# Kernel optimization log

Hardware: AMD Instinct MI355X
Metric: run time of the kernel (lower is better)

## Reference

```python
import jax, jax.numpy as jnp
import numpy as np

B, N, D = 2, 2048, 1024
H, DH = 16, 64
DI = 4096
EPS = 1e-5
NEG_SLOPE = 0.01  # F.leaky_relu default


def _ln(x, g, b):
    mu = jnp.mean(x, axis=-1, keepdims=True)
    var = jnp.mean((x - mu) ** 2, axis=-1, keepdims=True)
    return (x - mu) * jax.lax.rsqrt(var + EPS) * g + b


def setup_inputs() -> dict:
    key = jax.random.key(0)
    ks = jax.random.split(key, 10)
    s = 0.02
    return {
        "Z": jax.random.normal(ks[0], (B, N, D), jnp.float32),
        "new_mask": jax.random.normal(ks[1], (B, N, N), jnp.float32),
        "mask": jax.random.uniform(ks[2], (B, N, N), jnp.float32),
        "ln1_g": jnp.ones((D,), jnp.float32),
        "ln1_b": jnp.zeros((D,), jnp.float32),
        "qkv_w": jax.random.normal(ks[3], (3 * D, D), jnp.float32) * s,
        "qkv_b": jnp.zeros((3 * D,), jnp.float32),
        "o_w": jax.random.normal(ks[4], (D, H * DH), jnp.float32) * s,
        "ln2_g": jnp.ones((D,), jnp.float32),
        "ln2_b": jnp.zeros((D,), jnp.float32),
        "p1_w": jax.random.normal(ks[5], (DI, D), jnp.float32) * s,
        "p1_b": jnp.zeros((DI,), jnp.float32),
        "p2_w": jax.random.normal(ks[6], (D, DI), jnp.float32) * s,
        "p2_b": jnp.zeros((D,), jnp.float32),
    }


def reference(Z, new_mask, mask, ln1_g, ln1_b, qkv_w, qkv_b, o_w, ln2_g, ln2_b, p1_w, p1_b, p2_w, p2_b):
    inp = Z
    Zn = _ln(Z, ln1_g, ln1_b)
    qkv = (Zn @ qkv_w.T + qkv_b).reshape(B, N, H, 3 * DH)
    # torch chunk order in the source: V, Q, K
    V, Q, K = jnp.split(qkv, 3, axis=3)  # each [B,N,H,DH]
    # scores: einsum('bnij,bmij->binm') == [B,H,N,N]
    W = jnp.einsum("bnhd,bmhd->bhnm", Q, K) / np.sqrt(DH) + new_mask[:, None]
    A = jax.nn.softmax(W, axis=3) * mask[:, None]
    attn = jnp.einsum("bhnm,bmhd->bnhd", A, V).reshape(B, N, D)
    attn = jnp.where(attn >= 0, attn, NEG_SLOPE * attn) @ o_w.T  # leaky_relu then o_net (no bias)
    Z1 = attn + inp
    Zn2 = _ln(Z1, ln2_g, ln2_b)
    h = jax.nn.relu(Zn2 @ p1_w.T + p1_b)
    return h @ p2_w.T + p2_b + Z1
```

## Files before the change

### kernel.cpp

```cpp
#include <hip/hip_runtime.h>

typedef unsigned short u16;
typedef __attribute__((ext_vector_type(8))) short bf16x8;
typedef __attribute__((ext_vector_type(4))) float f32x4;

#define DEV static __device__ __forceinline__

DEV u16 f2bf(float f) {
    unsigned u = __float_as_uint(f);
    u += 0x7FFFu + ((u >> 16) & 1u);
    return (u16)(u >> 16);
}

typedef const __attribute__((address_space(1))) void* gas1_t;
typedef __attribute__((address_space(3))) void* gas3_t;

DEV void gl_lds16(const u16* g, u16* l) {
    __builtin_amdgcn_global_load_lds((gas1_t)g, (gas3_t)l, 16, 0, 0);
}

DEV int sw8(int row, int chunk) { return row * 64 + ((chunk ^ (row & 7)) << 3); }

__global__ __launch_bounds__(256) void prep_all(const float* __restrict__ qkv_w,
                                                const float* __restrict__ o_w,
                                                const float* __restrict__ p1_w,
                                                const float* __restrict__ p2_w,
                                                const float* __restrict__ qkv_b,
                                                const float* __restrict__ nm,
                                                const float* __restrict__ pm,
                                                u16* __restrict__ qkvW,
                                                u16* __restrict__ oW,
                                                u16* __restrict__ p1W,
                                                u16* __restrict__ p2W,
                                                float* __restrict__ pbias,
                                                unsigned* __restrict__ Mp) {
    const int bid = blockIdx.x, t = threadIdx.x;
    if (bid < 3072) {
        int i = bid * 256 + t;
        int orow = i >> 8, cc = i & 255;
        int region = orow >> 10, rem = orow & 1023, h = rem >> 6, tt = rem & 63;
        int srow = h * 192 + region * 64 + tt;
        float4 v = ((const float4*)qkv_w)[srow * 256 + cc];
        ushort4 o;
        o.x = f2bf(v.x); o.y = f2bf(v.y); o.z = f2bf(v.z); o.w = f2bf(v.w);
        ((ushort4*)qkvW)[i] = o;
    } else if (bid < 4096) {
        int i = (bid - 3072) * 256 + t;
        float4 v = ((const float4*)o_w)[i];
        ushort4 o;
        o.x = f2bf(v.x); o.y = f2bf(v.y); o.z = f2bf(v.z); o.w = f2bf(v.w);
        ((ushort4*)oW)[i] = o;
    } else if (bid < 8192) {
        int i = (bid - 4096) * 256 + t;
        float4 v = ((const float4*)p1_w)[i];
        ushort4 o;
        o.x = f2bf(v.x); o.y = f2bf(v.y); o.z = f2bf(v.z); o.w = f2bf(v.w);
        ((ushort4*)p1W)[i] = o;
    } else if (bid < 12288) {
        int i = (bid - 8192) * 256 + t;
        float4 v = ((const float4*)p2_w)[i];
        ushort4 o;
        o.x = f2bf(v.x); o.y = f2bf(v.y); o.z = f2bf(v.z); o.w = f2bf(v.w);
        ((ushort4*)p2W)[i] = o;
    } else if (bid < 20480) {
        int i = (bid - 12288) * 256 + t;
        float4 a = ((const float4*)nm)[i];
        float4 b = ((const float4*)pm)[i];
        uint4 o;
        o.x = ((unsigned)f2bf(b.x) << 16) | f2bf(a.x * 1.4426950f);
        o.y = ((unsigned)f2bf(b.y) << 16) | f2bf(a.y * 1.4426950f);
        o.z = ((unsigned)f2bf(b.z) << 16) | f2bf(a.z * 1.4426950f);
        o.w = ((unsigned)f2bf(b.w) << 16) | f2bf(a.w * 1.4426950f);
        ((uint4*)Mp)[i] = o;
    } else {
#pragma unroll
        for (int k = 0; k < 12; k++) {
            int i = k * 256 + t;
            int region = i >> 10, rem = i & 1023, h = rem >> 6, tt = rem & 63;
            pbias[i] = qkv_b[h * 192 + region * 64 + tt];
        }
    }
}

__global__ __launch_bounds__(256) void ln_bf16(const float* __restrict__ x,
                                               const float* __restrict__ gam,
                                               const float* __restrict__ bet,
                                               u16* __restrict__ y) {
    const int row = blockIdx.x;
    const int t = threadIdx.x;
    const float4 v = ((const float4*)(x + (size_t)row * 1024))[t];
    float s = v.x + v.y + v.z + v.w;
    float ss = v.x * v.x + v.y * v.y + v.z * v.z + v.w * v.w;
#pragma unroll
    for (int o = 1; o < 64; o <<= 1) {
        s += __shfl_xor(s, o);
        ss += __shfl_xor(ss, o);
    }
    __shared__ float rs[4], rss[4];
    const int wave = t >> 6, lane = t & 63;
    if (lane == 0) { rs[wave] = s; rss[wave] = ss; }
    __syncthreads();
    const float tot = rs[0] + rs[1] + rs[2] + rs[3];
    const float totss = rss[0] + rss[1] + rss[2] + rss[3];
    const float mu = tot * (1.0f / 1024.0f);
    const float var = totss * (1.0f / 1024.0f) - mu * mu;
    const float rstd = rsqrtf(var + 1e-5f);
    const float4 g4 = ((const float4*)gam)[t];
    const float4 b4 = ((const float4*)bet)[t];
    ushort4 o;
    o.x = f2bf((v.x - mu) * rstd * g4.x + b4.x);
    o.y = f2bf((v.y - mu) * rstd * g4.y + b4.y);
    o.z = f2bf((v.z - mu) * rstd * g4.z + b4.z);
    o.w = f2bf((v.w - mu) * rstd * g4.w + b4.w);
    ((ushort4*)(y + (size_t)row * 1024))[t] = o;
}

__global__ __launch_bounds__(256) void ln2_comb4(const float* __restrict__ p0,
                                                 const float* __restrict__ p1,
                                                 const float* __restrict__ p2,
                                                 const float* __restrict__ p3,
                                                 const float* __restrict__ Z,
                                                 const float* __restrict__ gam,
                                                 const float* __restrict__ bet,
                                                 float* __restrict__ Z1,
                                                 u16* __restrict__ y) {
    const int row = blockIdx.x;
    const int t = threadIdx.x;
    const size_t off = (size_t)row * 256 + t;
    const float4 a = ((const float4*)p0)[off];
    const float4 c = ((const float4*)p1)[off];
    const float4 d = ((const float4*)p2)[off];
    const float4 e = ((const float4*)p3)[off];
    const float4 z = ((const float4*)Z)[off];
    float4 v;
    v.x = a.x + c.x + d.x + e.x + z.x;
    v.y = a.y + c.y + d.y + e.y + z.y;
    v.z = a.z + c.z + d.z + e.z + z.z;
    v.w = a.w + c.w + d.w + e.w + z.w;
    ((float4*)Z1)[off] = v;
    float s = v.x + v.y + v.z + v.w;
    float ss = v.x * v.x + v.y * v.y + v.z * v.z + v.w * v.w;
#pragma unroll
    for (int o = 1; o < 64; o <<= 1) {
        s += __shfl_xor(s, o);
        ss += __shfl_xor(ss, o);
    }
    __shared__ float rs[4], rss[4];
    const int wave = t >> 6, lane = t & 63;
    if (lane == 0) { rs[wave] = s; rss[wave] = ss; }
    __syncthreads();
    const float tot = rs[0] + rs[1] + rs[2] + rs[3];
    const float totss = rss[0] + rss[1] + rss[2] + rss[3];
    const float mu = tot * (1.0f / 1024.0f);
    const float var = totss * (1.0f / 1024.0f) - mu * mu;
    const float rstd = rsqrtf(var + 1e-5f);
    const float4 g4 = ((const float4*)gam)[t];
    const float4 b4 = ((const float4*)bet)[t];
    ushort4 o;
    o.x = f2bf((v.x - mu) * rstd * g4.x + b4.x);
    o.y = f2bf((v.y - mu) * rstd * g4.y + b4.y);
    o.z = f2bf((v.z - mu) * rstd * g4.z + b4.z);
    o.w = f2bf((v.w - mu) * rstd * g4.w + b4.w);
    ((ushort4*)(y + (size_t)row * 1024))[t] = o;
}

__global__ __launch_bounds__(256) void out_comb(const float* __restrict__ p0,
                                                const float* __restrict__ p1,
                                                const float* __restrict__ bias,
                                                const float* __restrict__ Z1,
                                                float* __restrict__ out) {
    int i = blockIdx.x * 256 + threadIdx.x;
    float4 a = ((const float4*)p0)[i];
    float4 c = ((const float4*)p1)[i];
    float4 z = ((const float4*)Z1)[i];
    float4 b = ((const float4*)bias)[i & 255];
    float4 o;
    o.x = a.x + c.x + z.x + b.x; o.y = a.y + c.y + z.y + b.y;
    o.z = a.z + c.z + z.z + b.z; o.w = a.w + c.w + z.w + b.w;
    ((float4*)out)[i] = o;
}

template <int EPI>
__global__ __launch_bounds__(256, 3) void gemm_bt(const u16* __restrict__ A,
                                                  const u16* __restrict__ Bt,
                                                  const float* __restrict__ bias,
                                                  void* __restrict__ out0,
                                                  void* __restrict__ out1,
                                                  void* __restrict__ out2,
                                                  int M, int N, int K, int ldk) {
    __shared__ __align__(16) u16 As[128 * 32];
    __shared__ __align__(16) u16 Bs[128 * 32];
    const int tid = threadIdx.x;
    const int wave = tid >> 6, lane = tid & 63;
    const int lhi = lane >> 4, llo = lane & 15;
    const int bx = blockIdx.x, by = blockIdx.y;
    const int kz = blockIdx.z * K;

    const int arow = wave * 32 + (lane >> 2);
    const int acol = (lane & 3) * 8;
    const u16* gA = A + (size_t)(by * 128 + arow) * ldk + kz + acol;
    const u16* gB = Bt + (size_t)(bx * 128 + arow) * ldk + kz + acol;
    u16* lA = As + wave * 1024 + lane * 8;
    u16* lB = Bs + wave * 1024 + lane * 8;

    const int wr = wave >> 1, wc = wave & 1;
    const f32x4 zero = {0.f, 0.f, 0.f, 0.f};
    f32x4 acc[4][4];
#pragma unroll
    for (int i = 0; i < 4; i++)
#pragma unroll
        for (int j = 0; j < 4; j++) acc[i][j] = zero;

    for (int k0 = 0; k0 < K; k0 += 32) {
        __syncthreads();
        gl_lds16(gA, lA);
        gl_lds16(gA + 16 * (size_t)ldk, lA + 512);
        gl_lds16(gB, lB);
        gl_lds16(gB + 16 * (size_t)ldk, lB + 512);
        gA += 32; gB += 32;
        __syncthreads();
        bf16x8 af[4], bfr[4];
#pragma unroll
        for (int i = 0; i < 4; i++)
            af[i] = *(const bf16x8*)(As + (wr * 64 + i * 16 + llo) * 32 + lhi * 8);
#pragma unroll
        for (int j = 0; j < 4; j++)
            bfr[j] = *(const bf16x8*)(Bs + (wc * 64 + j * 16 + llo) * 32 + lhi * 8);
#pragma unroll
        for (int i = 0; i < 4; i++)
#pragma unroll
            for (int j = 0; j < 4; j++)
                acc[i][j] = __builtin_amdgcn_mfma_f32_16x16x32_bf16(af[i], bfr[j], acc[i][j], 0, 0, 0);
    }

    const int rbase = by * 128 + wr * 64 + lhi * 4;
    const int cbase = bx * 128 + wc * 64 + llo;
    float* pout = nullptr;
    if constexpr (EPI == 4) {
        pout = (blockIdx.z < 2) ? ((float*)out0 + (size_t)blockIdx.z * M * N)
                                : ((float*)out1 + (size_t)(blockIdx.z - 2) * M * N);
    }
#pragma unroll
    for (int i = 0; i < 4; i++) {
#pragma unroll
        for (int j = 0; j < 4; j++) {
#pragma unroll
            for (int r = 0; r < 4; r++) {
                const int row = rbase + i * 16 + r;
                const int col = cbase + j * 16;
                float v = acc[i][j][r];
                if constexpr (EPI == 0) {
                    v += bias[col];
                    const int region = col >> 10;
                    const int c = col & 1023;
                    const int b = row >> 11, n = row & 2047;
                    if (region == 0) {
                        ((float*)out0)[(size_t)row * 1024 + c] = v;
                    } else {
                        const int h = c >> 6, t = c & 63;
                        u16* dst = (region == 1) ? (u16*)out1 : (u16*)out2;
                        dst[(((size_t)(b * 16 + h)) * 2048 + n) * 64 + t] = f2bf(v);
                    }
                } else if constexpr (EPI == 2) {
                    v += bias[col];
                    v = v > 0.f ? v : 0.f;
                    ((u16*)out0)[(size_t)row * N + col] = f2bf(v);
                } else {
                    pout[(size_t)row * N + col] = v;
                }
            }
        }
    }
}

__global__ __launch_bounds__(256) void vtrans(const float* __restrict__ Vsc,
                                              u16* __restrict__ Vt) {
    __shared__ u16 Ts[64 * 72];
    const int nt = blockIdx.x;
    const int bh = blockIdx.y;
    const int b = bh >> 4, h = bh & 15;
    const int t = threadIdx.x;
    const int n0 = nt * 64;
    const int nr = t >> 2;
    const int dq = (t & 3) * 16;
    const float* src = Vsc + ((size_t)(b * 2048 + n0 + nr)) * 1024 + h * 64 + dq;
    float4 v0 = ((const float4*)src)[0];
    float4 v1 = ((const float4*)src)[1];
    float4 v2 = ((const float4*)src)[2];
    float4 v3 = ((const float4*)src)[3];
    u16* c0 = Ts + nr;
    c0[(dq + 0) * 72]  = f2bf(v0.x); c0[(dq + 1) * 72]  = f2bf(v0.y);
    c0[(dq + 2) * 72]  = f2bf(v0.z); c0[(dq + 3) * 72]  = f2bf(v0.w);
    c0[(dq + 4) * 72]  = f2bf(v1.x); c0[(dq + 5) * 72]  = f2bf(v1.y);
    c0[(dq + 6) * 72]  = f2bf(v1.z); c0[(dq + 7) * 72]  = f2bf(v1.w);
    c0[(dq + 8) * 72]  = f2bf(v2.x); c0[(dq + 9) * 72]  = f2bf(v2.y);
    c0[(dq + 10) * 72] = f2bf(v2.z); c0[(dq + 11) * 72] = f2bf(v2.w);
    c0[(dq + 12) * 72] = f2bf(v3.x); c0[(dq + 13) * 72] = f2bf(v3.y);
    c0[(dq + 14) * 72] = f2bf(v3.z); c0[(dq + 15) * 72] = f2bf(v3.w);
    __syncthreads();
    const int d = t >> 2, n8 = (t & 3) * 16;
    bf16x8 o0 = *(const bf16x8*)(Ts + d * 72 + n8);
    bf16x8 o1 = *(const bf16x8*)(Ts + d * 72 + n8 + 8);
    u16* dst = Vt + ((size_t)bh * 64 + d) * 2048 + n0 + n8;
    *(bf16x8*)dst = o0;
    *(bf16x8*)(dst + 8) = o1;
}

__global__ __launch_bounds__(256, 4) void attn_fused4(const u16* __restrict__ Qg,
                                                      const u16* __restrict__ Kg,
                                                      const u16* __restrict__ Vt,
                                                      const unsigned* __restrict__ Mp,
                                                      u16* __restrict__ attnL) {
    __shared__ __align__(16) u16 Qs[64 * 64];
    __shared__ __align__(16) u16 Ks[64 * 64];
    __shared__ __align__(16) u16 Vs[64 * 64];
    __shared__ __align__(16) u16 Ps[64 * 72];
    const int tid = threadIdx.x, wave = tid >> 6, lane = tid & 63;
    const int lhi = lane >> 4, llo = lane & 15;
    const int id = blockIdx.x;
    const int hh = id >> 6, rem = id & 63;
    const int b = rem >> 5, qt = rem & 31;
    const int bh = b * 16 + hh;
    const int q0 = qt * 64;
    const int l3 = lane >> 3, l7 = lane & 7;
    const int swcol = (l7 ^ (l3 & 7)) * 8;

#pragma unroll
    for (int s = 0; s < 2; s++) {
        const int row = wave * 16 + s * 8 + l3;
        gl_lds16(Qg + ((size_t)bh * 2048 + q0 + row) * 64 + swcol,
                 Qs + wave * 1024 + s * 512 + lane * 8);
    }

    const unsigned* Mpb = Mp + (size_t)b * 2048 * 2048;
    int midx[4];
#pragma unroll
    for (int r = 0; r < 4; r++)
        midx[r] = (q0 + wave * 16 + lhi * 4 + r) * 2048 + llo;

    const f32x4 zero = {0.f, 0.f, 0.f, 0.f};
    f32x4 accO[4];
    float lsum[4];
#pragma unroll
    for (int j = 0; j < 4; j++) accO[j] = zero;
#pragma unroll
    for (int r = 0; r < 4; r++) lsum[r] = 0.f;

    const float CS = 0.125f * 1.4426950f;
    const int pb0 = (wave * 16 + lhi * 4) * 72 + llo;

    for (int m0 = 0; m0 < 2048; m0 += 64) {
        __syncthreads();
#pragma unroll
        for (int s = 0; s < 2; s++) {
            const int row = wave * 16 + s * 8 + l3;
            gl_lds16(Kg + ((size_t)bh * 2048 + m0 + row) * 64 + swcol,
                     Ks + wave * 1024 + s * 512 + lane * 8);
            gl_lds16(Vt + ((size_t)bh * 64 + row) * 2048 + m0 + swcol,
                     Vs + wave * 1024 + s * 512 + lane * 8);
        }
        unsigned mv[4][4];
#pragma unroll
        for (int r = 0; r < 4; r++)
#pragma unroll
            for (int j = 0; j < 4; j++) mv[r][j] = Mpb[midx[r] + m0 + j * 16];
        __syncthreads();

        f32x4 sacc[4];
#pragma unroll
        for (int j = 0; j < 4; j++) sacc[j] = zero;
#pragma unroll
        for (int kk = 0; kk < 2; kk++) {
            const bf16x8 aq = *(const bf16x8*)(Qs + sw8(wave * 16 + llo, kk * 4 + lhi));
#pragma unroll
            for (int j = 0; j < 4; j++) {
                const bf16x8 bk = *(const bf16x8*)(Ks + sw8(j * 16 + llo, kk * 4 + lhi));
                sacc[j] = __builtin_amdgcn_mfma_f32_16x16x32_bf16(aq, bk, sacc[j], 0, 0, 0);
            }
        }

#pragma unroll
        for (int j = 0; j < 4; j++)
#pragma unroll
            for (int r = 0; r < 4; r++) {
                const unsigned u = mv[r][j];
                const float nm = __uint_as_float(u << 16);
                const float pm = __uint_as_float(u & 0xFFFF0000u);
                const float e = exp2f(fmaf(sacc[j][r], CS, nm));
                lsum[r] += e;
                const float p = e * pm;
                Ps[pb0 + r * 72 + j * 16] = (u16)(__float_as_uint(p) >> 16);
            }

#pragma unroll
        for (int kk = 0; kk < 2; kk++) {
            const bf16x8 ap = *(const bf16x8*)(Ps + (wave * 16 + llo) * 72 + kk * 32 + lhi * 8);
#pragma unroll
            for (int jd = 0; jd < 4; jd++) {
                const bf16x8 bv = *(const bf16x8*)(Vs + sw8(jd * 16 + llo, kk * 4 + lhi));
                accO[jd] = __builtin_amdgcn_mfma_f32_16x16x32_bf16(ap, bv, accO[jd], 0, 0, 0);
            }
        }
    }

#pragma unroll
    for (int r = 0; r < 4; r++) {
#pragma unroll
        for (int o = 1; o < 16; o <<= 1) lsum[r] += __shfl_xor(lsum[r], o);
        lsum[r] = 1.0f / lsum[r];
    }
#pragma unroll
    for (int jd = 0; jd < 4; jd++)
#pragma unroll
        for (int r = 0; r < 4; r++) {
            float v = accO[jd][r] * lsum[r];
            v = v >= 0.f ? v : 0.01f * v;
            const int q = q0 + wave * 16 + lhi * 4 + r;
            attnL[((size_t)b * 2048 + q) * 1024 + hh * 64 + jd * 16 + llo] = f2bf(v);
        }
}

extern "C" void kernel_launch(void* const* d_in, const int* in_sizes, int n_in,
                              void* d_out, int out_size, void* d_ws, size_t ws_size,
                              hipStream_t stream) {
    const float* Z     = (const float*)d_in[0];
    const float* nmask = (const float*)d_in[1];
    const float* pmask = (const float*)d_in[2];
    const float* ln1_g = (const float*)d_in[3];
    const float* ln1_b = (const float*)d_in[4];
    const float* qkv_w = (const float*)d_in[5];
    const float* qkv_b = (const float*)d_in[6];
    const float* o_w   = (const float*)d_in[7];
    const float* ln2_g = (const float*)d_in[8];
    const float* ln2_b = (const float*)d_in[9];
    const float* p1_w  = (const float*)d_in[10];
    const float* p1_b  = (const float*)d_in[11];
    const float* p2_w  = (const float*)d_in[12];
    const float* p2_b  = (const float*)d_in[13];
    float* out = (float*)d_out;

    char* w = (char*)d_ws;
    auto take = [&](size_t bytes) -> char* {
        char* p = w;
        w += (bytes + 255) & ~(size_t)255;
        return p;
    };
    u16* qkvW   = (u16*)take((size_t)3072 * 1024 * 2);
    u16* oW     = (u16*)take((size_t)1024 * 1024 * 2);
    u16* p1W    = (u16*)take((size_t)4096 * 1024 * 2);
    u16* p2W    = (u16*)take((size_t)1024 * 4096 * 2);
    u16* Zn     = (u16*)take((size_t)4096 * 1024 * 2);
    u16* Qb     = (u16*)take((size_t)32 * 2048 * 64 * 2);
    u16* Kb     = (u16*)take((size_t)32 * 2048 * 64 * 2);
    u16* Vt     = (u16*)take((size_t)32 * 64 * 2048 * 2);
    u16* attnL  = (u16*)take((size_t)4096 * 1024 * 2);
    float* Z1   = (float*)take((size_t)4096 * 1024 * 4);
    u16* hbuf   = (u16*)take((size_t)4096 * 4096 * 2);
    unsigned* Mp = (unsigned*)take((size_t)2 * 2048 * 2048 * 4);
    float* pbias = (float*)take((size_t)3072 * 4);
    float* Vsc    = (float*)hbuf;
    float* part01 = (float*)Mp;
    float* part23 = (float*)hbuf;

    prep_all<<<dim3(20481), 256, 0, stream>>>(qkv_w, o_w, p1_w, p2_w, qkv_b, nmask, pmask,
                                              qkvW, oW, p1W, p2W, pbias, Mp);
    ln_bf16<<<dim3(4096), 256, 0, stream>>>(Z, ln1_g, ln1_b, Zn);
    gemm_bt<0><<<dim3(24, 32), 256, 0, stream>>>(Zn, qkvW, pbias, Vsc, Qb, Kb, 4096, 3072, 1024, 1024);
    vtrans<<<dim3(32, 32), 256, 0, stream>>>(Vsc, Vt);
    attn_fused4<<<dim3(1024), 256, 0, stream>>>(Qb, Kb, Vt, Mp, attnL);
    gemm_bt<4><<<dim3(8, 32, 4), 256, 0, stream>>>(attnL, oW, nullptr, part01, part23, nullptr,
                                                   4096, 1024, 256, 1024);
    ln2_comb4<<<dim3(4096), 256, 0, stream>>>(part01, part01 + (size_t)4096 * 1024,
                                              part23, part23 + (size_t)4096 * 1024,
                                              Z, ln2_g, ln2_b, Z1, Zn);
    gemm_bt<2><<<dim3(32, 32), 256, 0, stream>>>(Zn, p1W, p1_b, hbuf, nullptr, nullptr,
                                                 4096, 4096, 1024, 1024);
    gemm_bt<4><<<dim3(8, 32, 2), 256, 0, stream>>>(hbuf, p2W, nullptr, part01, nullptr, nullptr,
                                                   4096, 1024, 2048, 4096);
    out_comb<<<dim3(4096), 256, 0, stream>>>(part01, part01 + (size_t)4096 * 1024, p2_b, Z1, out);
}
```

Baseline: 443.8 us.

## Fold LN1 into prep, transpose mask layout, fuse residual into o-proj GEMM

LayerNorm1 now runs inside the prep kernel, which removes one launch. The prep kernel also writes the packed mask transposed, so the attention kernel can load four query rows with one uint4 instead of scattered scalars. The o-projection drops its 4-way split-K and uses a 128x64 tile GEMM that adds the residual in its epilogue, removing the partial-sum combine kernel. V is now written as bf16 to cut vtrans traffic, and the attention exp uses the hardware exp2 builtin. The transposed mask write needs an extra LDS transpose, and the o-proj GEMM now runs a full K loop per block with less parallelism.

```diff
diff --git a/kernel.cpp b/kernel.cpp
--- a/kernel.cpp
+++ b/kernel.cpp
@@ -21,74 +21,8 @@
 
 DEV int sw8(int row, int chunk) { return row * 64 + ((chunk ^ (row & 7)) << 3); }
 
-__global__ __launch_bounds__(256) void prep_all(const float* __restrict__ qkv_w,
-                                                const float* __restrict__ o_w,
-                                                const float* __restrict__ p1_w,
-                                                const float* __restrict__ p2_w,
-                                                const float* __restrict__ qkv_b,
-                                                const float* __restrict__ nm,
-                                                const float* __restrict__ pm,
-                                                u16* __restrict__ qkvW,
-                                                u16* __restrict__ oW,
-                                                u16* __restrict__ p1W,
-                                                u16* __restrict__ p2W,
-                                                float* __restrict__ pbias,
-                                                unsigned* __restrict__ Mp) {
-    const int bid = blockIdx.x, t = threadIdx.x;
-    if (bid < 3072) {
-        int i = bid * 256 + t;
-        int orow = i >> 8, cc = i & 255;
-        int region = orow >> 10, rem = orow & 1023, h = rem >> 6, tt = rem & 63;
-        int srow = h * 192 + region * 64 + tt;
-        float4 v = ((const float4*)qkv_w)[srow * 256 + cc];
-        ushort4 o;
-        o.x = f2bf(v.x); o.y = f2bf(v.y); o.z = f2bf(v.z); o.w = f2bf(v.w);
-        ((ushort4*)qkvW)[i] = o;
-    } else if (bid < 4096) {
-        int i = (bid - 3072) * 256 + t;
-        float4 v = ((const float4*)o_w)[i];
-        ushort4 o;
-        o.x = f2bf(v.x); o.y = f2bf(v.y); o.z = f2bf(v.z); o.w = f2bf(v.w);
-        ((ushort4*)oW)[i] = o;
-    } else if (bid < 8192) {
-        int i = (bid - 4096) * 256 + t;
-        float4 v = ((const float4*)p1_w)[i];
-        ushort4 o;
-        o.x = f2bf(v.x); o.y = f2bf(v.y); o.z = f2bf(v.z); o.w = f2bf(v.w);
-        ((ushort4*)p1W)[i] = o;
-    } else if (bid < 12288) {
-        int i = (bid - 8192) * 256 + t;
-        float4 v = ((const float4*)p2_w)[i];
-        ushort4 o;
-        o.x = f2bf(v.x); o.y = f2bf(v.y); o.z = f2bf(v.z); o.w = f2bf(v.w);
-        ((ushort4*)p2W)[i] = o;
-    } else if (bid < 20480) {
-        int i = (bid - 12288) * 256 + t;
-        float4 a = ((const float4*)nm)[i];
-        float4 b = ((const float4*)pm)[i];
-        uint4 o;
-        o.x = ((unsigned)f2bf(b.x) << 16) | f2bf(a.x * 1.4426950f);
-        o.y = ((unsigned)f2bf(b.y) << 16) | f2bf(a.y * 1.4426950f);
-        o.z = ((unsigned)f2bf(b.z) << 16) | f2bf(a.z * 1.4426950f);
-        o.w = ((unsigned)f2bf(b.w) << 16) | f2bf(a.w * 1.4426950f);
-        ((uint4*)Mp)[i] = o;
-    } else {
-#pragma unroll
-        for (int k = 0; k < 12; k++) {
-            int i = k * 256 + t;
-            int region = i >> 10, rem = i & 1023, h = rem >> 6, tt = rem & 63;
-            pbias[i] = qkv_b[h * 192 + region * 64 + tt];
-        }
-    }
-}
-
-__global__ __launch_bounds__(256) void ln_bf16(const float* __restrict__ x,
-                                               const float* __restrict__ gam,
-                                               const float* __restrict__ bet,
-                                               u16* __restrict__ y) {
-    const int row = blockIdx.x;
-    const int t = threadIdx.x;
-    const float4 v = ((const float4*)(x + (size_t)row * 1024))[t];
+DEV void ln_body(const float4 v, const float* gam, const float* bet, float* shm,
+                 int t, u16* yrow) {
     float s = v.x + v.y + v.z + v.w;
     float ss = v.x * v.x + v.y * v.y + v.z * v.z + v.w * v.w;
 #pragma unroll
@@ -96,7 +30,8 @@
         s += __shfl_xor(s, o);
         ss += __shfl_xor(ss, o);
     }
-    __shared__ float rs[4], rss[4];
+    float* rs = shm;
+    float* rss = shm + 4;
     const int wave = t >> 6, lane = t & 63;
     if (lane == 0) { rs[wave] = s; rss[wave] = ss; }
     __syncthreads();
@@ -112,56 +47,104 @@
     o.y = f2bf((v.y - mu) * rstd * g4.y + b4.y);
     o.z = f2bf((v.z - mu) * rstd * g4.z + b4.z);
     o.w = f2bf((v.w - mu) * rstd * g4.w + b4.w);
-    ((ushort4*)(y + (size_t)row * 1024))[t] = o;
-}
-
-__global__ __launch_bounds__(256) void ln2_comb4(const float* __restrict__ p0,
-                                                 const float* __restrict__ p1,
-                                                 const float* __restrict__ p2,
-                                                 const float* __restrict__ p3,
-                                                 const float* __restrict__ Z,
-                                                 const float* __restrict__ gam,
-                                                 const float* __restrict__ bet,
-                                                 float* __restrict__ Z1,
-                                                 u16* __restrict__ y) {
-    const int row = blockIdx.x;
-    const int t = threadIdx.x;
-    const size_t off = (size_t)row * 256 + t;
-    const float4 a = ((const float4*)p0)[off];
-    const float4 c = ((const float4*)p1)[off];
-    const float4 d = ((const float4*)p2)[off];
-    const float4 e = ((const float4*)p3)[off];
-    const float4 z = ((const float4*)Z)[off];
-    float4 v;
-    v.x = a.x + c.x + d.x + e.x + z.x;
-    v.y = a.y + c.y + d.y + e.y + z.y;
-    v.z = a.z + c.z + d.z + e.z + z.z;
-    v.w = a.w + c.w + d.w + e.w + z.w;
-    ((float4*)Z1)[off] = v;
-    float s = v.x + v.y + v.z + v.w;
-    float ss = v.x * v.x + v.y * v.y + v.z * v.z + v.w * v.w;
-#pragma unroll
-    for (int o = 1; o < 64; o <<= 1) {
-        s += __shfl_xor(s, o);
-        ss += __shfl_xor(ss, o);
-    }
-    __shared__ float rs[4], rss[4];
-    const int wave = t >> 6, lane = t & 63;
-    if (lane == 0) { rs[wave] = s; rss[wave] = ss; }
-    __syncthreads();
-    const float tot = rs[0] + rs[1] + rs[2] + rs[3];
-    const float totss = rss[0] + rss[1] + rss[2] + rss[3];
-    const float mu = tot * (1.0f / 1024.0f);
-    const float var = totss * (1.0f / 1024.0f) - mu * mu;
-    const float rstd = rsqrtf(var + 1e-5f);
-    const float4 g4 = ((const float4*)gam)[t];
-    const float4 b4 = ((const float4*)bet)[t];
-    ushort4 o;
-    o.x = f2bf((v.x - mu) * rstd * g4.x + b4.x);
-    o.y = f2bf((v.y - mu) * rstd * g4.y + b4.y);
-    o.z = f2bf((v.z - mu) * rstd * g4.z + b4.z);
-    o.w = f2bf((v.w - mu) * rstd * g4.w + b4.w);
-    ((ushort4*)(y + (size_t)row * 1024))[t] = o;
+    ((ushort4*)yrow)[t] = o;
+}
+
+__global__ __launch_bounds__(256) void prep_all(const float* __restrict__ Z,
+                                                const float* __restrict__ ln1_g,
+                                                const float* __restrict__ ln1_b,
+                                                const float* __restrict__ qkv_w,
+                                                const float* __restrict__ o_w,
+                                                const float* __restrict__ p1_w,
+                                                const float* __restrict__ p2_w,
+                                                const float* __restrict__ qkv_b,
+                                                const float* __restrict__ nm,
+                                                const float* __restrict__ pm,
+                                                u16* __restrict__ Zn,
+                                                u16* __restrict__ qkvW,
+                                                u16* __restrict__ oW,
+                                                u16* __restrict__ p1W,
+                                                u16* __restrict__ p2W,
+                                                float* __restrict__ pbias,
+                                                unsigned* __restrict__ Mpt) {
+    __shared__ unsigned T[64 * 65];
+    const int bid = blockIdx.x, t = threadIdx.x;
+    if (bid < 4096) {
+        const float4 v = ((const float4*)(Z + (size_t)bid * 1024))[t];
+        ln_body(v, ln1_g, ln1_b, (float*)T, t, Zn + (size_t)bid * 1024);
+    } else if (bid < 7168) {
+        int i = (bid - 4096) * 256 + t;
+        int orow = i >> 8, cc = i & 255;
+        int region = orow >> 10, rem = orow & 1023, h = rem >> 6, tt = rem & 63;
+        int srow = h * 192 + region * 64 + tt;
+        float4 v = ((const float4*)qkv_w)[srow * 256 + cc];
+        ushort4 o;
+        o.x = f2bf(v.x); o.y = f2bf(v.y); o.z = f2bf(v.z); o.w = f2bf(v.w);
+        ((ushort4*)qkvW)[i] = o;
+    } else if (bid < 8192) {
+        int i = (bid - 7168) * 256 + t;
+        float4 v = ((const float4*)o_w)[i];
+        ushort4 o;
+        o.x = f2bf(v.x); o.y = f2bf(v.y); o.z = f2bf(v.z); o.w = f2bf(v.w);
+        ((ushort4*)oW)[i] = o;
+    } else if (bid < 12288) {
+        int i = (bid - 8192) * 256 + t;
+        float4 v = ((const float4*)p1_w)[i];
+        ushort4 o;
+        o.x = f2bf(v.x); o.y = f2bf(v.y); o.z = f2bf(v.z); o.w = f2bf(v.w);
+        ((ushort4*)p1W)[i] = o;
+    } else if (bid < 16384) {
+        int i = (bid - 12288) * 256 + t;
+        float4 v = ((const float4*)p2_w)[i];
+        ushort4 o;
+        o.x = f2bf(v.x); o.y = f2bf(v.y); o.z = f2bf(v.z); o.w = f2bf(v.w);
+        ((ushort4*)p2W)[i] = o;
+    } else if (bid < 18432) {
+        int bid2 = bid - 16384;
+        int b = bid2 >> 10, rem = bid2 & 1023, qt = rem >> 5, mt = rem & 31;
+        const size_t base = (size_t)b * 2048 * 2048;
+        const int tq = t >> 4, tm4 = (t & 15) * 4;
+#pragma unroll
+        for (int s = 0; s < 4; s++) {
+            const int q = qt * 64 + s * 16 + tq;
+            const size_t off = base + (size_t)q * 2048 + mt * 64 + tm4;
+            const float4 a = *(const float4*)(nm + off);
+            const float4 p = *(const float4*)(pm + off);
+            unsigned* row = T + (s * 16 + tq);
+            row[(tm4 + 0) * 65] = ((unsigned)f2bf(p.x) << 16) | f2bf(a.x * 1.4426950f);
+            row[(tm4 + 1) * 65] = ((unsigned)f2bf(p.y) << 16) | f2bf(a.y * 1.4426950f);
+            row[(tm4 + 2) * 65] = ((unsigned)f2bf(p.z) << 16) | f2bf(a.z * 1.4426950f);
+            row[(tm4 + 3) * 65] = ((unsigned)f2bf(p.w) << 16) | f2bf(a.w * 1.4426950f);
+        }
+        __syncthreads();
+#pragma unroll
+        for (int s = 0; s < 4; s++) {
+            const int ml = s * 16 + tq;
+            uint4 o;
+            o.x = T[ml * 65 + tm4 + 0];
+            o.y = T[ml * 65 + tm4 + 1];
+            o.z = T[ml * 65 + tm4 + 2];
+            o.w = T[ml * 65 + tm4 + 3];
+            *(uint4*)(Mpt + base + (size_t)(mt * 64 + ml) * 2048 + qt * 64 + tm4) = o;
+        }
+    } else {
+#pragma unroll
+        for (int k = 0; k < 12; k++) {
+            int i = k * 256 + t;
+            int region = i >> 10, rem = i & 1023, h = rem >> 6, tt = rem & 63;
+            pbias[i] = qkv_b[h * 192 + region * 64 + tt];
+        }
+    }
+}
+
+__global__ __launch_bounds__(256) void ln_bf16(const float* __restrict__ x,
+                                               const float* __restrict__ gam,
+                                               const float* __restrict__ bet,
+                                               u16* __restrict__ y) {
+    __shared__ float shm[8];
+    const int row = blockIdx.x, t = threadIdx.x;
+    const float4 v = ((const float4*)(x + (size_t)row * 1024))[t];
+    ln_body(v, gam, bet, shm, t, y + (size_t)row * 1024);
 }
 
 __global__ __launch_bounds__(256) void out_comb(const float* __restrict__ p0,
@@ -180,34 +163,38 @@
     ((float4*)out)[i] = o;
 }
 
-template <int EPI>
+template <int EPI, int BN>
 __global__ __launch_bounds__(256, 3) void gemm_bt(const u16* __restrict__ A,
                                                   const u16* __restrict__ Bt,
                                                   const float* __restrict__ bias,
+                                                  const float* __restrict__ res,
                                                   void* __restrict__ out0,
                                                   void* __restrict__ out1,
                                                   void* __restrict__ out2,
                                                   int M, int N, int K, int ldk) {
+    constexpr int RT = (BN == 128) ? 4 : 2;
     __shared__ __align__(16) u16 As[128 * 32];
-    __shared__ __align__(16) u16 Bs[128 * 32];
+    __shared__ __align__(16) u16 Bs[BN * 32];
     const int tid = threadIdx.x;
     const int wave = tid >> 6, lane = tid & 63;
     const int lhi = lane >> 4, llo = lane & 15;
     const int bx = blockIdx.x, by = blockIdx.y;
     const int kz = blockIdx.z * K;
+    const int wr = (BN == 128) ? (wave >> 1) : wave;
+    const int wc = (BN == 128) ? (wave & 1) : 0;
 
     const int arow = wave * 32 + (lane >> 2);
     const int acol = (lane & 3) * 8;
     const u16* gA = A + (size_t)(by * 128 + arow) * ldk + kz + acol;
-    const u16* gB = Bt + (size_t)(bx * 128 + arow) * ldk + kz + acol;
     u16* lA = As + wave * 1024 + lane * 8;
-    u16* lB = Bs + wave * 1024 + lane * 8;
-
-    const int wr = wave >> 1, wc = wave & 1;
+    const int brow = (BN == 128) ? arow : (wave * 16 + (lane >> 2));
+    const u16* gB = Bt + (size_t)(bx * BN + brow) * ldk + kz + acol;
+    u16* lB = Bs + ((BN == 128) ? wave * 1024 : wave * 512) + lane * 8;
+
     const f32x4 zero = {0.f, 0.f, 0.f, 0.f};
-    f32x4 acc[4][4];
-#pragma unroll
-    for (int i = 0; i < 4; i++)
+    f32x4 acc[RT][4];
+#pragma unroll
+    for (int i = 0; i < RT; i++)
 #pragma unroll
         for (int j = 0; j < 4; j++) acc[i][j] = zero;
 
@@ -216,32 +203,28 @@
         gl_lds16(gA, lA);
         gl_lds16(gA + 16 * (size_t)ldk, lA + 512);
         gl_lds16(gB, lB);
-        gl_lds16(gB + 16 * (size_t)ldk, lB + 512);
+        if (BN == 128) gl_lds16(gB + 16 * (size_t)ldk, lB + 512);
         gA += 32; gB += 32;
         __syncthreads();
-        bf16x8 af[4], bfr[4];
-#pragma unroll
-        for (int i = 0; i < 4; i++)
-            af[i] = *(const bf16x8*)(As + (wr * 64 + i * 16 + llo) * 32 + lhi * 8);
+        bf16x8 af[RT], bfr[4];
+#pragma unroll
+        for (int i = 0; i < RT; i++)
+            af[i] = *(const bf16x8*)(As + (wr * (RT * 16) + i * 16 + llo) * 32 + lhi * 8);
 #pragma unroll
         for (int j = 0; j < 4; j++)
             bfr[j] = *(const bf16x8*)(Bs + (wc * 64 + j * 16 + llo) * 32 + lhi * 8);
 #pragma unroll
-        for (int i = 0; i < 4; i++)
+        for (int i = 0; i < RT; i++)
 #pragma unroll
             for (int j = 0; j < 4; j++)
                 acc[i][j] = __builtin_amdgcn_mfma_f32_16x16x32_bf16(af[i], bfr[j], acc[i][j], 0, 0, 0);
     }
 
-    const int rbase = by * 128 + wr * 64 + lhi * 4;
-    const int cbase = bx * 128 + wc * 64 + llo;
-    float* pout = nullptr;
-    if constexpr (EPI == 4) {
-        pout = (blockIdx.z < 2) ? ((float*)out0 + (size_t)blockIdx.z * M * N)
-                                : ((float*)out1 + (size_t)(blockIdx.z - 2) * M * N);
-    }
-#pragma unroll
-    for (int i = 0; i < 4; i++) {
+    const int rbase = by * 128 + wr * (RT * 16) + lhi * 4;
+    const int cbase = bx * BN + wc * 64 + llo;
+    float* pout = (EPI == 4) ? ((float*)out0 + (size_t)blockIdx.z * M * N) : (float*)out0;
+#pragma unroll
+    for (int i = 0; i < RT; i++) {
 #pragma unroll
         for (int j = 0; j < 4; j++) {
 #pragma unroll
@@ -255,12 +238,14 @@
                     const int c = col & 1023;
                     const int b = row >> 11, n = row & 2047;
                     if (region == 0) {
-                        ((float*)out0)[(size_t)row * 1024 + c] = v;
+                        ((u16*)out0)[(size_t)row * 1024 + c] = f2bf(v);
                     } else {
-                        const int h = c >> 6, t = c & 63;
+                        const int h = c >> 6, tt = c & 63;
                         u16* dst = (region == 1) ? (u16*)out1 : (u16*)out2;
-                        dst[(((size_t)(b * 16 + h)) * 2048 + n) * 64 + t] = f2bf(v);
+                        dst[(((size_t)(b * 16 + h)) * 2048 + n) * 64 + tt] = f2bf(v);
                     }
+                } else if constexpr (EPI == 1) {
+                    ((float*)out0)[(size_t)row * N + col] = v + res[(size_t)row * N + col];
                 } else if constexpr (EPI == 2) {
                     v += bias[col];
                     v = v > 0.f ? v : 0.f;
@@ -273,7 +258,7 @@
     }
 }
 
-__global__ __launch_bounds__(256) void vtrans(const float* __restrict__ Vsc,
+__global__ __launch_bounds__(256) void vtrans(const u16* __restrict__ Vsc,
                                               u16* __restrict__ Vt) {
     __shared__ u16 Ts[64 * 72];
     const int nt = blockIdx.x;
@@ -283,20 +268,14 @@
     const int n0 = nt * 64;
     const int nr = t >> 2;
     const int dq = (t & 3) * 16;
-    const float* src = Vsc + ((size_t)(b * 2048 + n0 + nr)) * 1024 + h * 64 + dq;
-    float4 v0 = ((const float4*)src)[0];
-    float4 v1 = ((const float4*)src)[1];
-    float4 v2 = ((const float4*)src)[2];
-    float4 v3 = ((const float4*)src)[3];
+    const u16* src = Vsc + ((size_t)(b * 2048 + n0 + nr)) * 1024 + h * 64 + dq;
+    bf16x8 a0 = *(const bf16x8*)src;
+    bf16x8 a1 = *(const bf16x8*)(src + 8);
     u16* c0 = Ts + nr;
-    c0[(dq + 0) * 72]  = f2bf(v0.x); c0[(dq + 1) * 72]  = f2bf(v0.y);
-    c0[(dq + 2) * 72]  = f2bf(v0.z); c0[(dq + 3) * 72]  = f2bf(v0.w);
-    c0[(dq + 4) * 72]  = f2bf(v1.x); c0[(dq + 5) * 72]  = f2bf(v1.y);
-    c0[(dq + 6) * 72]  = f2bf(v1.z); c0[(dq + 7) * 72]  = f2bf(v1.w);
-    c0[(dq + 8) * 72]  = f2bf(v2.x); c0[(dq + 9) * 72]  = f2bf(v2.y);
-    c0[(dq + 10) * 72] = f2bf(v2.z); c0[(dq + 11) * 72] = f2bf(v2.w);
-    c0[(dq + 12) * 72] = f2bf(v3.x); c0[(dq + 13) * 72] = f2bf(v3.y);
-    c0[(dq + 14) * 72] = f2bf(v3.z); c0[(dq + 15) * 72] = f2bf(v3.w);
+#pragma unroll
+    for (int k = 0; k < 8; k++) c0[(dq + k) * 72] = (u16)a0[k];
+#pragma unroll
+    for (int k = 0; k < 8; k++) c0[(dq + 8 + k) * 72] = (u16)a1[k];
     __syncthreads();
     const int d = t >> 2, n8 = (t & 3) * 16;
     bf16x8 o0 = *(const bf16x8*)(Ts + d * 72 + n8);
@@ -306,10 +285,10 @@
     *(bf16x8*)(dst + 8) = o1;
 }
 
-__global__ __launch_bounds__(256, 4) void attn_fused4(const u16* __restrict__ Qg,
+__global__ __launch_bounds__(256, 4) void attn_fused5(const u16* __restrict__ Qg,
                                                       const u16* __restrict__ Kg,
                                                       const u16* __restrict__ Vt,
-                                                      const unsigned* __restrict__ Mp,
+                                                      const unsigned* __restrict__ Mpt,
                                                       u16* __restrict__ attnL) {
     __shared__ __align__(16) u16 Qs[64 * 64];
     __shared__ __align__(16) u16 Ks[64 * 64];
@@ -332,11 +311,8 @@
                  Qs + wave * 1024 + s * 512 + lane * 8);
     }
 
-    const unsigned* Mpb = Mp + (size_t)b * 2048 * 2048;
-    int midx[4];
-#pragma unroll
-    for (int r = 0; r < 4; r++)
-        midx[r] = (q0 + wave * 16 + lhi * 4 + r) * 2048 + llo;
+    const unsigned* Mb = Mpt + (size_t)b * 2048 * 2048 + (size_t)llo * 2048 +
+                         (q0 + wave * 16 + lhi * 4);
 
     const f32x4 zero = {0.f, 0.f, 0.f, 0.f};
     f32x4 accO[4];
@@ -359,11 +335,10 @@
             gl_lds16(Vt + ((size_t)bh * 64 + row) * 2048 + m0 + swcol,
                      Vs + wave * 1024 + s * 512 + lane * 8);
         }
-        unsigned mv[4][4];
-#pragma unroll
-        for (int r = 0; r < 4; r++)
-#pragma unroll
-            for (int j = 0; j < 4; j++) mv[r][j] = Mpb[midx[r] + m0 + j * 16];
+        uint4 mv[4];
+#pragma unroll
+        for (int j = 0; j < 4; j++)
+            mv[j] = *(const uint4*)(Mb + (size_t)(m0 + j * 16) * 2048);
         __syncthreads();
 
         f32x4 sacc[4];
@@ -380,17 +355,19 @@
         }
 
 #pragma unroll
-        for (int j = 0; j < 4; j++)
+        for (int j = 0; j < 4; j++) {
+            const unsigned* mj = (const unsigned*)&mv[j];
 #pragma unroll
             for (int r = 0; r < 4; r++) {
-                const unsigned u = mv[r][j];
+                const unsigned u = mj[r];
                 const float nm = __uint_as_float(u << 16);
                 const float pm = __uint_as_float(u & 0xFFFF0000u);
-                const float e = exp2f(fmaf(sacc[j][r], CS, nm));
+                const float e = __builtin_amdgcn_exp2f(fmaf(sacc[j][r], CS, nm));
                 lsum[r] += e;
                 const float p = e * pm;
                 Ps[pb0 + r * 72 + j * 16] = (u16)(__float_as_uint(p) >> 16);
             }
+        }
 
 #pragma unroll
         for (int kk = 0; kk < 2; kk++) {
@@ -456,26 +433,24 @@
     u16* attnL  = (u16*)take((size_t)4096 * 1024 * 2);
     float* Z1   = (float*)take((size_t)4096 * 1024 * 4);
     u16* hbuf   = (u16*)take((size_t)4096 * 4096 * 2);
-    unsigned* Mp = (unsigned*)take((size_t)2 * 2048 * 2048 * 4);
+    unsigned* Mpt = (unsigned*)take((size_t)2 * 2048 * 2048 * 4);
     float* pbias = (float*)take((size_t)3072 * 4);
-    float* Vsc    = (float*)hbuf;
-    float* part01 = (float*)Mp;
-    float* part23 = (float*)hbuf;
-
-    prep_all<<<dim3(20481), 256, 0, stream>>>(qkv_w, o_w, p1_w, p2_w, qkv_b, nmask, pmask,
-                                              qkvW, oW, p1W, p2W, pbias, Mp);
-    ln_bf16<<<dim3(4096), 256, 0, stream>>>(Z, ln1_g, ln1_b, Zn);
-    gemm_bt<0><<<dim3(24, 32), 256, 0, stream>>>(Zn, qkvW, pbias, Vsc, Qb, Kb, 4096, 3072, 1024, 1024);
+    u16* Vsc      = (u16*)hbuf;
+    float* part01 = (float*)Mpt;
+
+    prep_all<<<dim3(18433), 256, 0, stream>>>(Z, ln1_g, ln1_b, qkv_w, o_w, p1_w, p2_w,
+                                              qkv_b, nmask, pmask,
+                                              Zn, qkvW, oW, p1W, p2W, pbias, Mpt);
+    gemm_bt<0, 128><<<dim3(24, 32), 256, 0, stream>>>(Zn, qkvW, pbias, nullptr,
+                                                      Vsc, Qb, Kb, 4096, 3072, 1024, 1024);
     vtrans<<<dim3(32, 32), 256, 0, stream>>>(Vsc, Vt);
-    attn_fused4<<<dim3(1024), 256, 0, stream>>>(Qb, Kb, Vt, Mp, attnL);
-    gemm_bt<4><<<dim3(8, 32, 4), 256, 0, stream>>>(attnL, oW, nullptr, part01, part23, nullptr,
-                                                   4096, 1024, 256, 1024);
-    ln2_comb4<<<dim3(4096), 256, 0, stream>>>(part01, part01 + (size_t)4096 * 1024,
-                                              part23, part23 + (size_t)4096 * 1024,
-                                              Z, ln2_g, ln2_b, Z1, Zn);
-    gemm_bt<2><<<dim3(32, 32), 256, 0, stream>>>(Zn, p1W, p1_b, hbuf, nullptr, nullptr,
-                                                 4096, 4096, 1024, 1024);
-    gemm_bt<4><<<dim3(8, 32, 2), 256, 0, stream>>>(hbuf, p2W, nullptr, part01, nullptr, nullptr,
-                                                   4096, 1024, 2048, 4096);
+    attn_fused5<<<dim3(1024), 256, 0, stream>>>(Qb, Kb, Vt, Mpt, attnL);
+    gemm_bt<1, 64><<<dim3(16, 32), 256, 0, stream>>>(attnL, oW, nullptr, Z,
+                                                     Z1, nullptr, nullptr, 4096, 1024, 1024, 1024);
+    ln_bf16<<<dim3(4096), 256, 0, stream>>>(Z1, ln2_g, ln2_b, Zn);
+    gemm_bt<2, 128><<<dim3(32, 32), 256, 0, stream>>>(Zn, p1W, p1_b, nullptr,
+                                                      hbuf, nullptr, nullptr, 4096, 4096, 1024, 1024);
+    gemm_bt<4, 128><<<dim3(8, 32, 2), 256, 0, stream>>>(hbuf, p2W, nullptr, nullptr,
+                                                        part01, nullptr, nullptr, 4096, 1024, 2048, 4096);
     out_comb<<<dim3(4096), 256, 0, stream>>>(part01, part01 + (size_t)4096 * 1024, p2_b, Z1, out);
 }
```

Result: slower. 453.8 us (+2.3%).
